# Kernel tuning notes

Hardware: AMD Instinct MI355X
Metric: run time of the kernel (lower is better)

The kernel has to match this reference:

```python
import jax, jax.numpy as jnp
import numpy as np

IN_C, C_M, C_N, K = 512, 512, 128, 1
B, H, W = 8, 64, 64

def setup_inputs() -> dict:
    key = jax.random.key(0)
    ks = jax.random.split(key, 8)
    s = 1.0 / np.sqrt(IN_C)
    return {
        "x": jax.random.normal(ks[0], (B, IN_C, H, W), dtype=jnp.float32),
        "y": jax.random.normal(ks[1], (B, C_M, H, W), dtype=jnp.float32),
        "wA": jax.random.uniform(ks[2], (C_M, IN_C), minval=-s, maxval=s, dtype=jnp.float32),
        "bA": jax.random.uniform(ks[3], (C_M,), minval=-s, maxval=s, dtype=jnp.float32),
        "wB": jax.random.uniform(ks[4], (C_N, IN_C), minval=-s, maxval=s, dtype=jnp.float32),
        "bB": jax.random.uniform(ks[5], (C_N,), minval=-s, maxval=s, dtype=jnp.float32),
        "wV": jax.random.uniform(ks[6], (C_N, IN_C), minval=-s, maxval=s, dtype=jnp.float32),
        "bV": jax.random.uniform(ks[7], (C_N,), minval=-s, maxval=s, dtype=jnp.float32),
    }

def reference(x, y, wA, bA, wB, bB, wV, bV):
    # A2-Net double attention, K=1 so batch = b1 and K*h*w = N.
    b, c, h, w = x.shape
    N = h * w
    xf = x.reshape(b, c, N)                                  # [b, C, N]
    A = jnp.einsum('mc,bcn->bmn', wA, xf) + bA[:, None]      # [b, c_m, N]
    Bf = jnp.einsum('kc,bcn->bkn', wB, xf) + bB[:, None]     # [b, c_n, N]
    V = jnp.einsum('kc,bcn->bkn', wV, xf) + bV[:, None]      # [b, c_n, N]
    # tmpB viewed (b*c_n, N), softmax dim=1 -> softmax over N per (b, c_n) row
    softB = jax.nn.softmax(Bf, axis=-1)                      # [b, c_n, N]
    # tmpV viewed (b*N, c_n), softmax dim=1 -> softmax over c_n per pixel
    softV = jax.nn.softmax(V, axis=1)                        # [b, c_n, N]
    # gather: tmpG = tmpA @ softB^T  -> [b, c_m, c_n]
    G = jnp.einsum('bmn,bkn->bmk', A, softB)
    # distribute: tmpZ = G @ softV -> [b, c_m, N]
    Z = jnp.einsum('bmk,bkn->bmn', G, softV)
    return Z.reshape(b, -1, h, w) + y
```

## Files before the change

### kernel.cpp

```cpp
#include <hip/hip_runtime.h>

#define BATCH 8
#define INC 512
#define CM 512
#define CN 128
#define NPIX 4096
#define NSPLIT 8

typedef short bf16x8 __attribute__((ext_vector_type(8)));
typedef float f32x4 __attribute__((ext_vector_type(4)));
typedef unsigned short us8v __attribute__((ext_vector_type(8)));

__device__ __forceinline__ unsigned short f2b(float f) {
    union { float f; unsigned u; } v; v.f = f;
    unsigned r = v.u + 0x7FFF + ((v.u >> 16) & 1);
    return (unsigned short)(r >> 16);
}
__device__ __forceinline__ float b2f(unsigned short u) {
    union { unsigned u; float f; } v; v.u = ((unsigned)u) << 16;
    return v.f;
}

__device__ __forceinline__ void gl_lds16(const unsigned short* g, unsigned short* l) {
    __builtin_amdgcn_global_load_lds(
        (const __attribute__((address_space(1))) unsigned int*)g,
        (__attribute__((address_space(3))) unsigned int*)l, 16, 0, 0);
}

__device__ __forceinline__ void stage_tile(const unsigned short* src, int ld, int kbase,
                                           unsigned short* lds, int t) {
    #pragma unroll
    for (int q = 0; q < 2; ++q) {
        int f = q * 256 + t;
        const unsigned short* g = src + (size_t)(f >> 2) * ld + kbase + (f & 3) * 8;
        gl_lds16(g, lds + f * 8);
    }
}

__device__ __forceinline__ void bt_compute(const unsigned short* lA, const unsigned short* lB,
                                           f32x4 acc[4][4], int wr, int wc, int lane) {
    int lr = lane & 15, lq = lane >> 4;
    bf16x8 av[4], bv[4];
    #pragma unroll
    for (int i = 0; i < 4; ++i)
        av[i] = *(const bf16x8*)&lA[(wr * 64 + i * 16 + lr) * 32 + lq * 8];
    #pragma unroll
    for (int j = 0; j < 4; ++j)
        bv[j] = *(const bf16x8*)&lB[(wc * 64 + j * 16 + lr) * 32 + lq * 8];
    #pragma unroll
    for (int i = 0; i < 4; ++i)
        #pragma unroll
        for (int j = 0; j < 4; ++j)
            acc[i][j] = __builtin_amdgcn_mfma_f32_16x16x32_bf16(av[i], bv[j], acc[i][j], 0, 0, 0);
}

#define ZERO_ACC(acc)                       \
    f32x4 acc[4][4];                        \
    {                                       \
        f32x4 z4 = {0.f, 0.f, 0.f, 0.f};   \
        for (int i = 0; i < 4; ++i)         \
            for (int j = 0; j < 4; ++j)     \
                acc[i][j] = z4;             \
    }

__device__ __forceinline__ void pipe_loop(const unsigned short* A, int lda,
                                          const unsigned short* Bm, int ldb,
                                          int kbase, int nt,
                                          unsigned short* lds, f32x4 acc[4][4],
                                          int t, int wr, int wc, int lane)
{
    stage_tile(A, lda, kbase, lds, t);
    stage_tile(Bm, ldb, kbase, lds + 4096, t);
    __syncthreads();
    int cur = 0;
    for (int it = 0; it < nt - 1; ++it) {
        unsigned short* nb = lds + ((cur ^ 1) << 13);
        stage_tile(A, lda, kbase + (it + 1) * 32, nb, t);
        stage_tile(Bm, ldb, kbase + (it + 1) * 32, nb + 4096, t);
        bt_compute(lds + (cur << 13), lds + (cur << 13) + 4096, acc, wr, wc, lane);
        __syncthreads();
        cur ^= 1;
    }
    bt_compute(lds + (cur << 13), lds + (cur << 13) + 4096, acc, wr, wc, lane);
}

__global__ __launch_bounds__(256) void k_prep(
    const float* __restrict__ x, const float* __restrict__ wA,
    const float* __restrict__ wB, const float* __restrict__ wV,
    unsigned short* __restrict__ xT, unsigned short* __restrict__ x16,
    unsigned short* __restrict__ wA16, unsigned short* __restrict__ wB16,
    unsigned short* __restrict__ wV16)
{
    if (blockIdx.z == BATCH) {
        int bl = blockIdx.y * 64 + blockIdx.x;
        if (bl >= 384) return;
        int e = (bl * 256 + threadIdx.x) * 4;
        const float* src; unsigned short* dst; int off;
        if (e < 262144)       { src = wA; dst = wA16; off = e; }
        else if (e < 327680)  { src = wB; dst = wB16; off = e - 262144; }
        else                  { src = wV; dst = wV16; off = e - 327680; }
        float4 v = *(const float4*)&src[off];
        *(ushort4*)&dst[off] = make_ushort4(f2b(v.x), f2b(v.y), f2b(v.z), f2b(v.w));
        return;
    }
    __shared__ unsigned short tile[64][68];
    int n0 = blockIdx.x * 64, c0 = blockIdx.y * 64, b = blockIdx.z;
    int t = threadIdx.x;
    int tr = t >> 4, tc4 = (t & 15) * 4;
    const float* xb = x + ((size_t)b * INC + c0) * NPIX + n0;
    unsigned short* x16p = x16 + ((size_t)b * INC + c0) * NPIX + n0;
    #pragma unroll
    for (int p = 0; p < 4; ++p) {
        int r = p * 16 + tr;
        float4 v = *(const float4*)&xb[(size_t)r * NPIX + tc4];
        ushort4 u = make_ushort4(f2b(v.x), f2b(v.y), f2b(v.z), f2b(v.w));
        *(ushort4*)&x16p[(size_t)r * NPIX + tc4] = u;
        tile[r][tc4 + 0] = u.x; tile[r][tc4 + 1] = u.y;
        tile[r][tc4 + 2] = u.z; tile[r][tc4 + 3] = u.w;
    }
    __syncthreads();
    unsigned short* o = xT + ((size_t)b * NPIX + n0) * INC + c0;
    #pragma unroll
    for (int p = 0; p < 4; ++p) {
        int n = p * 16 + tr;
        ushort4 u = make_ushort4(tile[tc4 + 0][n], tile[tc4 + 1][n],
                                 tile[tc4 + 2][n], tile[tc4 + 3][n]);
        *(ushort4*)&o[(size_t)n * INC + tc4] = u;
    }
}

__global__ __launch_bounds__(256) void k_proj(
    const unsigned short* __restrict__ xT, const unsigned short* __restrict__ wB16,
    const unsigned short* __restrict__ wV16, const float* __restrict__ bB,
    const float* __restrict__ bV, unsigned short* __restrict__ Bf16,
    unsigned short* __restrict__ V16)
{
    __shared__ __align__(16) unsigned short lds[16384];
    int t = threadIdx.x;
    int n0 = blockIdx.x * 128;
    int z = blockIdx.y, b = z >> 1, br = z & 1;
    const unsigned short* A = br ? wV16 : wB16;
    const float* bias = br ? bV : bB;
    unsigned short* out = br ? V16 : Bf16;
    const unsigned short* Bm = xT + ((size_t)b * NPIX + n0) * INC;

    ZERO_ACC(acc);
    int lane = t & 63, w = t >> 6, wr = w >> 1, wc = w & 1;

    pipe_loop(A, INC, Bm, INC, 0, INC / 32, lds, acc, t, wr, wc, lane);

    int lr = lane & 15, lq = lane >> 4;
    int r0 = wr * 64 + lq * 4;
    unsigned short* op = out + (size_t)b * CN * NPIX + n0 + wc * 64 + lr;
    #pragma unroll
    for (int i = 0; i < 4; ++i)
        #pragma unroll
        for (int reg = 0; reg < 4; ++reg) {
            int k = r0 + i * 16 + reg;
            float bv_ = bias[k];
            #pragma unroll
            for (int j = 0; j < 4; ++j)
                op[(size_t)k * NPIX + j * 16] = f2b(acc[i][j][reg] + bv_);
        }
}

__global__ __launch_bounds__(256) void k_softmax_rows(
    const unsigned short* __restrict__ Bf16, unsigned short* __restrict__ sB)
{
    __shared__ float red[8];
    int row = blockIdx.x, t = threadIdx.x;
    const unsigned short* p = Bf16 + (size_t)row * NPIX + t * 16;
    us8v u0 = *(const us8v*)p, u1 = *(const us8v*)(p + 8);
    float v[16];
    #pragma unroll
    for (int j = 0; j < 8; ++j) { v[j] = b2f(u0[j]); v[8 + j] = b2f(u1[j]); }
    float m = -1e30f;
    #pragma unroll
    for (int j = 0; j < 16; ++j) m = fmaxf(m, v[j]);
    for (int o = 32; o > 0; o >>= 1) m = fmaxf(m, __shfl_xor(m, o));
    if ((t & 63) == 0) red[t >> 6] = m;
    __syncthreads();
    m = fmaxf(fmaxf(red[0], red[1]), fmaxf(red[2], red[3]));
    float s = 0.f;
    #pragma unroll
    for (int j = 0; j < 16; ++j) { v[j] = __expf(v[j] - m); s += v[j]; }
    for (int o = 32; o > 0; o >>= 1) s += __shfl_xor(s, o);
    if ((t & 63) == 0) red[4 + (t >> 6)] = s;
    __syncthreads();
    float r = 1.0f / (red[4] + red[5] + red[6] + red[7]);
    us8v o0, o1;
    #pragma unroll
    for (int j = 0; j < 8; ++j) { o0[j] = f2b(v[j] * r); o1[j] = f2b(v[8 + j] * r); }
    unsigned short* q = sB + (size_t)row * NPIX + t * 16;
    *(us8v*)q = o0; *(us8v*)(q + 8) = o1;
}

__global__ __launch_bounds__(256) void k_softmax_cols(
    const unsigned short* __restrict__ V16, unsigned short* __restrict__ sVt)
{
    __shared__ unsigned short tv[128][138];
    __shared__ float pm[2][128], ps[2][128], sm[128], sr[128];
    int n0 = blockIdx.x * 128, b = blockIdx.y, t = threadIdx.x;
    const unsigned short* vb = V16 + (size_t)b * CN * NPIX + n0;
    #pragma unroll
    for (int it = 0; it < 8; ++it) {
        int f = it * 256 + t, k = f >> 4, n8 = (f & 15) * 8;
        us8v u = *(const us8v*)&vb[(size_t)k * NPIX + n8];
        #pragma unroll
        for (int j = 0; j < 8; ++j) tv[n8 + j][k] = u[j];
    }
    __syncthreads();
    {
        int p = t & 127, h = t >> 7;
        float m = -1e30f;
        for (int k = h * 64; k < h * 64 + 64; ++k) m = fmaxf(m, b2f(tv[p][k]));
        float s = 0.f;
        for (int k = h * 64; k < h * 64 + 64; ++k) s += __expf(b2f(tv[p][k]) - m);
        pm[h][p] = m; ps[h][p] = s;
    }
    __syncthreads();
    if (t < 128) {
        float ma = pm[0][t], mb = pm[1][t];
        float m = fmaxf(ma, mb);
        float s = ps[0][t] * __expf(ma - m) + ps[1][t] * __expf(mb - m);
        sm[t] = m; sr[t] = 1.0f / s;
    }
    __syncthreads();
    unsigned short* ob = sVt + ((size_t)b * NPIX + n0) * CN;
    #pragma unroll
    for (int it = 0; it < 8; ++it) {
        int idx = it * 2048 + t * 8, nl = idx >> 7, k0 = idx & 127;
        float m = sm[nl], r = sr[nl];
        us8v o;
        #pragma unroll
        for (int j = 0; j < 8; ++j) o[j] = f2b(__expf(b2f(tv[nl][k0 + j]) - m) * r);
        *(us8v*)&ob[(size_t)nl * CN + k0] = o;
    }
}

__global__ __launch_bounds__(256) void k_gather(
    const unsigned short* __restrict__ x16, const unsigned short* __restrict__ sB,
    float* __restrict__ Pts)
{
    __shared__ __align__(16) unsigned short lds[16384];
    int t = threadIdx.x;
    int c0 = blockIdx.x * 128, s = blockIdx.y, b = blockIdx.z;
    const unsigned short* A = sB + (size_t)b * CN * NPIX;
    const unsigned short* Bm = x16 + ((size_t)b * INC + c0) * NPIX;
    int nbase = s * (NPIX / NSPLIT);

    ZERO_ACC(acc);
    int lane = t & 63, w = t >> 6, wr = w >> 1, wc = w & 1;

    pipe_loop(A, NPIX, Bm, NPIX, nbase, (NPIX / NSPLIT) / 32, lds, acc, t, wr, wc, lane);

    int lr = lane & 15, lq = lane >> 4;
    int r0 = wr * 64 + lq * 4;
    float* op = Pts + ((size_t)s * BATCH + b) * CN * INC + c0 + wc * 64 + lr;
    #pragma unroll
    for (int i = 0; i < 4; ++i)
        #pragma unroll
        for (int reg = 0; reg < 4; ++reg) {
            int k = r0 + i * 16 + reg;
            #pragma unroll
            for (int j = 0; j < 4; ++j)
                op[(size_t)k * INC + j * 16] = acc[i][j][reg];
        }
}

__global__ __launch_bounds__(256) void k_reduceP(
    const float* __restrict__ Pts, unsigned short* __restrict__ Pt16)
{
    int base = (blockIdx.x * 256 + threadIdx.x) * 4;
    float4 sacc = make_float4(0.f, 0.f, 0.f, 0.f);
    #pragma unroll
    for (int sp = 0; sp < NSPLIT; ++sp) {
        float4 v = *(const float4*)&Pts[(size_t)sp * (BATCH * CN * INC) + base];
        sacc.x += v.x; sacc.y += v.y; sacc.z += v.z; sacc.w += v.w;
    }
    *(ushort4*)&Pt16[base] = make_ushort4(f2b(sacc.x), f2b(sacc.y), f2b(sacc.z), f2b(sacc.w));
}

__global__ __launch_bounds__(256) void k_G(
    const unsigned short* __restrict__ wA16, const float* __restrict__ bA,
    const unsigned short* __restrict__ Pt16, unsigned short* __restrict__ G16)
{
    __shared__ __align__(16) unsigned short lds[16384];
    int t = threadIdx.x;
    int m0 = blockIdx.x * 128, b = blockIdx.y;
    const unsigned short* A = wA16 + (size_t)m0 * INC;
    const unsigned short* Bm = Pt16 + (size_t)b * CN * INC;

    ZERO_ACC(acc);
    int lane = t & 63, w = t >> 6, wr = w >> 1, wc = w & 1;

    pipe_loop(A, INC, Bm, INC, 0, INC / 32, lds, acc, t, wr, wc, lane);

    int lr = lane & 15, lq = lane >> 4;
    int r0 = wr * 64 + lq * 4;
    unsigned short* op = G16 + ((size_t)b * CM + m0) * CN + wc * 64 + lr;
    #pragma unroll
    for (int i = 0; i < 4; ++i)
        #pragma unroll
        for (int reg = 0; reg < 4; ++reg) {
            int mloc = r0 + i * 16 + reg;
            float bv_ = bA[m0 + mloc];
            #pragma unroll
            for (int j = 0; j < 4; ++j)
                op[(size_t)mloc * CN + j * 16] = f2b(acc[i][j][reg] + bv_);
        }
}

__global__ __launch_bounds__(256) void k_Z(
    const unsigned short* __restrict__ G16, const unsigned short* __restrict__ sVt,
    const float* __restrict__ y, float* __restrict__ out)
{
    __shared__ __align__(16) unsigned short lds[16384];
    int t = threadIdx.x;
    int n0 = blockIdx.x * 128, m0 = blockIdx.y * 128, b = blockIdx.z;
    const unsigned short* A = G16 + ((size_t)b * CM + m0) * CN;
    const unsigned short* Bm = sVt + ((size_t)b * NPIX + n0) * CN;

    ZERO_ACC(acc);
    int lane = t & 63, w = t >> 6, wr = w >> 1, wc = w & 1;

    pipe_loop(A, CN, Bm, CN, 0, CN / 32, lds, acc, t, wr, wc, lane);

    int lr = lane & 15, lq = lane >> 4;
    size_t rbase = ((size_t)b * CM + m0 + wr * 64 + lq * 4) * NPIX + n0 + wc * 64 + lr;
    #pragma unroll
    for (int i = 0; i < 4; ++i)
        #pragma unroll
        for (int reg = 0; reg < 4; ++reg) {
            size_t ro = rbase + (size_t)(i * 16 + reg) * NPIX;
            #pragma unroll
            for (int j = 0; j < 4; ++j)
                out[ro + j * 16] = acc[i][j][reg] + y[ro + j * 16];
        }
}

extern "C" void kernel_launch(void* const* d_in, const int* in_sizes, int n_in,
                              void* d_out, int out_size, void* d_ws, size_t ws_size,
                              hipStream_t stream)
{
    const float* x  = (const float*)d_in[0];
    const float* y  = (const float*)d_in[1];
    const float* wA = (const float*)d_in[2];
    const float* bA = (const float*)d_in[3];
    const float* wB = (const float*)d_in[4];
    const float* bB = (const float*)d_in[5];
    const float* wV = (const float*)d_in[6];
    const float* bV = (const float*)d_in[7];
    float* out = (float*)d_out;

    unsigned short* xT16 = (unsigned short*)d_ws;
    unsigned short* x16  = xT16 + 16777216;
    unsigned short* wA16 = x16  + 16777216;
    unsigned short* wB16 = wA16 + 262144;
    unsigned short* wV16 = wB16 + 65536;
    unsigned short* Bf16 = wV16 + 65536;
    unsigned short* V16  = Bf16 + 4194304;
    unsigned short* sB   = V16  + 4194304;
    unsigned short* sVt  = sB   + 4194304;
    unsigned short* Pt16 = sVt  + 4194304;
    float*  Pts = (float*)(Pt16 + 524288);
    unsigned short* G16  = (unsigned short*)(Pts + (size_t)NSPLIT * BATCH * CN * INC);

    k_prep<<<dim3(64, 8, BATCH + 1), 256, 0, stream>>>(
        x, wA, wB, wV, xT16, x16, wA16, wB16, wV16);
    k_proj<<<dim3(NPIX / 128, BATCH * 2), 256, 0, stream>>>(
        xT16, wB16, wV16, bB, bV, Bf16, V16);
    k_softmax_rows<<<dim3(BATCH * CN), 256, 0, stream>>>(Bf16, sB);
    k_softmax_cols<<<dim3(NPIX / 128, BATCH), 256, 0, stream>>>(V16, sVt);
    k_gather<<<dim3(INC / 128, NSPLIT, BATCH), 256, 0, stream>>>(x16, sB, Pts);
    k_reduceP<<<512, 256, 0, stream>>>(Pts, Pt16);
    k_G<<<dim3(CM / 128, BATCH), 256, 0, stream>>>(wA16, bA, Pt16, G16);
    k_Z<<<dim3(NPIX / 128, CM / 128, BATCH), 256, 0, stream>>>(G16, sVt, y, out);
}
```

Measured before the change: 253.3 us.

## Fuse B/V projections into one kernel sharing x tiles; prefetch y in k_Z

k_proj now computes both the B and V projections in one block over a 64-pixel tile. The x tile is staged once and reused for both weight matrices, so x is read from global memory half as often, and the block runs its own double-buffered pipeline. k_Z gets an explicit double-buffered loop and loads half of its y residual tile into registers before the MMA loop, to hide that load latency. The cost is higher register and LDS use per block, and a different grid shape for k_proj.

```diff
diff --git a/kernel.cpp b/kernel.cpp
--- a/kernel.cpp
+++ b/kernel.cpp
@@ -37,6 +37,12 @@
     }
 }
 
+__device__ __forceinline__ void stage_half(const unsigned short* src, int ld, int kbase,
+                                           unsigned short* lds, int t) {
+    const unsigned short* g = src + (size_t)(t >> 2) * ld + kbase + (t & 3) * 8;
+    gl_lds16(g, lds + t * 8);
+}
+
 __device__ __forceinline__ void bt_compute(const unsigned short* lA, const unsigned short* lB,
                                            f32x4 acc[4][4], int wr, int wc, int lane) {
     int lr = lane & 15, lq = lane >> 4;
@@ -52,6 +58,29 @@
         #pragma unroll
         for (int j = 0; j < 4; ++j)
             acc[i][j] = __builtin_amdgcn_mfma_f32_16x16x32_bf16(av[i], bv[j], acc[i][j], 0, 0, 0);
+}
+
+__device__ __forceinline__ void bt2_compute(const unsigned short* lA0, const unsigned short* lA1,
+                                            const unsigned short* lBx,
+                                            f32x4 aB[4][2], f32x4 aV[4][2],
+                                            int wr, int wc, int lane) {
+    int lr = lane & 15, lq = lane >> 4;
+    bf16x8 a0[4], a1[4], bv[2];
+    #pragma unroll
+    for (int i = 0; i < 4; ++i) {
+        a0[i] = *(const bf16x8*)&lA0[(wr * 64 + i * 16 + lr) * 32 + lq * 8];
+        a1[i] = *(const bf16x8*)&lA1[(wr * 64 + i * 16 + lr) * 32 + lq * 8];
+    }
+    #pragma unroll
+    for (int j = 0; j < 2; ++j)
+        bv[j] = *(const bf16x8*)&lBx[(wc * 32 + j * 16 + lr) * 32 + lq * 8];
+    #pragma unroll
+    for (int i = 0; i < 4; ++i)
+        #pragma unroll
+        for (int j = 0; j < 2; ++j) {
+            aB[i][j] = __builtin_amdgcn_mfma_f32_16x16x32_bf16(a0[i], bv[j], aB[i][j], 0, 0, 0);
+            aV[i][j] = __builtin_amdgcn_mfma_f32_16x16x32_bf16(a1[i], bv[j], aV[i][j], 0, 0, 0);
+        }
 }
 
 #define ZERO_ACC(acc)                       \
@@ -135,32 +164,53 @@
     const float* __restrict__ bV, unsigned short* __restrict__ Bf16,
     unsigned short* __restrict__ V16)
 {
-    __shared__ __align__(16) unsigned short lds[16384];
+    __shared__ __align__(16) unsigned short lds[20480];
     int t = threadIdx.x;
-    int n0 = blockIdx.x * 128;
-    int z = blockIdx.y, b = z >> 1, br = z & 1;
-    const unsigned short* A = br ? wV16 : wB16;
-    const float* bias = br ? bV : bB;
-    unsigned short* out = br ? V16 : Bf16;
-    const unsigned short* Bm = xT + ((size_t)b * NPIX + n0) * INC;
-
-    ZERO_ACC(acc);
+    int n0 = blockIdx.x * 64, b = blockIdx.y;
+    const unsigned short* Bx = xT + ((size_t)b * NPIX + n0) * INC;
+
+    f32x4 accB[4][2], accV[4][2];
+    {
+        f32x4 z4 = {0.f, 0.f, 0.f, 0.f};
+        for (int i = 0; i < 4; ++i)
+            for (int j = 0; j < 2; ++j) { accB[i][j] = z4; accV[i][j] = z4; }
+    }
     int lane = t & 63, w = t >> 6, wr = w >> 1, wc = w & 1;
-
-    pipe_loop(A, INC, Bm, INC, 0, INC / 32, lds, acc, t, wr, wc, lane);
-
-    int lr = lane & 15, lq = lane >> 4;
+    int lr = lane & 15, lq = lane >> 4;
+
+    stage_tile(wB16, INC, 0, lds, t);
+    stage_tile(wV16, INC, 0, lds + 4096, t);
+    stage_half(Bx, INC, 0, lds + 8192, t);
+    __syncthreads();
+    int cur = 0;
+    for (int it = 0; it < 15; ++it) {
+        unsigned short* nb = lds + (cur ^ 1) * 10240;
+        int c = (it + 1) * 32;
+        stage_tile(wB16, INC, c, nb, t);
+        stage_tile(wV16, INC, c, nb + 4096, t);
+        stage_half(Bx, INC, c, nb + 8192, t);
+        const unsigned short* cb = lds + cur * 10240;
+        bt2_compute(cb, cb + 4096, cb + 8192, accB, accV, wr, wc, lane);
+        __syncthreads();
+        cur ^= 1;
+    }
+    {
+        const unsigned short* cb = lds + cur * 10240;
+        bt2_compute(cb, cb + 4096, cb + 8192, accB, accV, wr, wc, lane);
+    }
     int r0 = wr * 64 + lq * 4;
-    unsigned short* op = out + (size_t)b * CN * NPIX + n0 + wc * 64 + lr;
     #pragma unroll
     for (int i = 0; i < 4; ++i)
         #pragma unroll
         for (int reg = 0; reg < 4; ++reg) {
             int k = r0 + i * 16 + reg;
-            float bv_ = bias[k];
-            #pragma unroll
-            for (int j = 0; j < 4; ++j)
-                op[(size_t)k * NPIX + j * 16] = f2b(acc[i][j][reg] + bv_);
+            float vB = bB[k], vV = bV[k];
+            size_t rowo = ((size_t)b * CN + k) * NPIX + n0 + wc * 32 + lr;
+            #pragma unroll
+            for (int j = 0; j < 2; ++j) {
+                Bf16[rowo + j * 16] = f2b(accB[i][j][reg] + vB);
+                V16 [rowo + j * 16] = f2b(accV[i][j][reg] + vV);
+            }
         }
 }
 
@@ -323,13 +373,42 @@
 
     ZERO_ACC(acc);
     int lane = t & 63, w = t >> 6, wr = w >> 1, wc = w & 1;
-
-    pipe_loop(A, CN, Bm, CN, 0, CN / 32, lds, acc, t, wr, wc, lane);
-
     int lr = lane & 15, lq = lane >> 4;
     size_t rbase = ((size_t)b * CM + m0 + wr * 64 + lq * 4) * NPIX + n0 + wc * 64 + lr;
-    #pragma unroll
-    for (int i = 0; i < 4; ++i)
+
+    stage_tile(A, CN, 0, lds, t);
+    stage_tile(Bm, CN, 0, lds + 4096, t);
+    float yA[2][4][4];
+    #pragma unroll
+    for (int i = 0; i < 2; ++i)
+        #pragma unroll
+        for (int reg = 0; reg < 4; ++reg)
+            #pragma unroll
+            for (int j = 0; j < 4; ++j)
+                yA[i][reg][j] = y[rbase + (size_t)(i * 16 + reg) * NPIX + j * 16];
+    __syncthreads();
+    int cur = 0;
+    for (int it = 0; it < 3; ++it) {
+        unsigned short* nb = lds + ((cur ^ 1) << 13);
+        stage_tile(A, CN, (it + 1) * 32, nb, t);
+        stage_tile(Bm, CN, (it + 1) * 32, nb + 4096, t);
+        bt_compute(lds + (cur << 13), lds + (cur << 13) + 4096, acc, wr, wc, lane);
+        __syncthreads();
+        cur ^= 1;
+    }
+    bt_compute(lds + (cur << 13), lds + (cur << 13) + 4096, acc, wr, wc, lane);
+
+    #pragma unroll
+    for (int i = 0; i < 2; ++i)
+        #pragma unroll
+        for (int reg = 0; reg < 4; ++reg) {
+            size_t ro = rbase + (size_t)(i * 16 + reg) * NPIX;
+            #pragma unroll
+            for (int j = 0; j < 4; ++j)
+                out[ro + j * 16] = acc[i][j][reg] + yA[i][reg][j];
+        }
+    #pragma unroll
+    for (int i = 2; i < 4; ++i)
         #pragma unroll
         for (int reg = 0; reg < 4; ++reg) {
             size_t ro = rbase + (size_t)(i * 16 + reg) * NPIX;
@@ -368,7 +447,7 @@
 
     k_prep<<<dim3(64, 8, BATCH + 1), 256, 0, stream>>>(
         x, wA, wB, wV, xT16, x16, wA16, wB16, wV16);
-    k_proj<<<dim3(NPIX / 128, BATCH * 2), 256, 0, stream>>>(
+    k_proj<<<dim3(NPIX / 64, BATCH), 256, 0, stream>>>(
         xT16, wB16, wV16, bB, bV, Bf16, V16);
     k_softmax_rows<<<dim3(BATCH * CN), 256, 0, stream>>>(Bf16, sB);
     k_softmax_cols<<<dim3(NPIX / 128, BATCH), 256, 0, stream>>>(V16, sVt);
```

Result: no change. 253.7 us (+0.1%).
